# Performance work log

Hardware: AMD Instinct MI355X
Metric: run time of the kernel (lower is better)

Reference implementation:

```python
import jax, jax.numpy as jnp
import numpy as np

B, S, D, H, AD, E = 4, 2048, 1024, 2048, 128, 8

def _ln(x, g, b, eps=1e-5):
    m = jnp.mean(x, axis=-1, keepdims=True)
    v = jnp.var(x, axis=-1, keepdims=True)
    return (x - m) * jax.lax.rsqrt(v + eps) * g + b

def setup_inputs() -> dict:
    key = jax.random.key(0)
    ks = jax.random.split(key, 12)
    scale = 1.0 / D ** 0.5
    ascale = scale * 0.01
    ead = 0.01 / AD ** 0.5
    return {
        'x': jax.random.normal(ks[0], (B, S, D), jnp.float32),
        'expert_weights': jax.random.uniform(ks[1], (B, S, E), jnp.float32),
        'Wu': jax.random.normal(ks[2], (H, D), jnp.float32) * scale,
        'bu': jnp.zeros((H,), jnp.float32),
        'Wg': jax.random.normal(ks[3], (H, D), jnp.float32) * scale,
        'bg': jnp.zeros((H,), jnp.float32),
        'Wd': jax.random.normal(ks[4], (D, H), jnp.float32) * scale,
        'bd': jnp.zeros((D,), jnp.float32),
        'Wpre': jax.random.normal(ks[5], (AD, D), jnp.float32) * ascale,
        'bpre': jnp.zeros((AD,), jnp.float32),
        'Wpost': jax.random.normal(ks[6], (AD, H), jnp.float32) * ascale,
        'bpost': jnp.zeros((AD,), jnp.float32),
        'ln_g': jnp.ones((AD,), jnp.float32),
        'ln_b': jnp.zeros((AD,), jnp.float32),
        'Wap': jax.random.normal(ks[7], (H, AD), jnp.float32) * ascale,
        'A': jax.random.normal(ks[8], (E, AD, AD), jnp.float32) * ead,
        'eg': jnp.ones((E, AD), jnp.float32),
        'eb': jnp.zeros((E, AD), jnp.float32),
        'Wp': jax.random.normal(ks[9], (H, AD), jnp.float32) * ead,
        'Wo': jax.random.normal(ks[10], (D, H), jnp.float32) * ead,
    }

def reference(x, expert_weights, Wu, bu, Wg, bg, Wd, bd, Wpre, bpre, Wpost, bpost, ln_g, ln_b, Wap, A, eg, eb, Wp, Wo):
    # ---- SharedExpertMLP ----
    up = x @ Wu.T + bu                      # [B,S,H]
    gate = x @ Wg.T + bg
    hidden = jax.nn.silu(gate) * up
    adapt_in = _ln(x @ Wpre.T + bpre, ln_g, ln_b)        # [B,S,AD]
    adapt_out = _ln(hidden @ Wpost.T + bpost, ln_g, ln_b)
    aw = jnp.einsum('bsa,bta->bst', adapt_in, adapt_out)  # [B,S,S]
    aw = jax.nn.silu(jnp.clip(aw, -5.0, 5.0))
    adapt = jnp.einsum('bst,bta->bsa', aw, adapt_in)
    hidden = hidden + 0.1 * (adapt @ Wap.T)
    shared = hidden @ Wd.T + bd                           # [B,S,D]
    # ---- expert branch (vectorized over experts) ----
    pre = x @ Wpre.T + bpre                               # [B,S,AD] (no adapt_norm here, as in torch)
    h = jnp.einsum('bsa,eca->ebsc', pre, A)               # per-expert adapter linear
    h = _ln(h, eg[:, None, None, :], eb[:, None, None, :])
    wmask = jnp.where(expert_weights > 0, expert_weights, 0.0)  # [B,S,E]
    hw = jnp.einsum('ebsa,bse->bsa', h, wmask)            # weighted combine before shared projections
    Wc = Wo @ Wp                                          # [D,AD]: output_proj(expert_proj(.))
    contrib = hw @ Wc.T                                   # [B,S,D]
    # sum_i w_i * (shared + 0.1*mask_i*expert_i) = shared*sum(w) + 0.1*sum(w_i*expert_i)
    return shared * jnp.sum(expert_weights, axis=-1, keepdims=True) + 0.1 * contrib
```

## Files before the change

kernel.cpp:

```cpp
#include <hip/hip_runtime.h>
#include <math.h>

#define BB 4
#define SS 2048
#define DD 1024
#define HH 2048
#define AD 128
#define EE 8
#define MM (BB*SS)

typedef unsigned short u16;
typedef short bf16x8 __attribute__((ext_vector_type(8)));
typedef float f32x4 __attribute__((ext_vector_type(4)));

__device__ __forceinline__ float silu_f(float x){ return x / (1.f + __expf(-x)); }

__device__ __forceinline__ u16 f2bf(float f){
    union { float f; unsigned u; } c; c.f = f;
    unsigned r = (c.u + 0x7FFFu + ((c.u >> 16) & 1u)) >> 16;
    return (u16)r;
}
__device__ __forceinline__ float bf2f(u16 u){
    union { unsigned u; float f; } c; c.u = ((unsigned)u) << 16;
    return c.f;
}

__device__ __forceinline__ void gld16(const u16* g, u16* l){
    __builtin_amdgcn_global_load_lds((const __attribute__((address_space(1))) void*)g,
                                     (__attribute__((address_space(3))) void*)l, 16, 0, 0);
}

template<int EPI>
__global__ __launch_bounds__(256,2) void mfma_nt(
    const u16* __restrict__ A, const u16* __restrict__ B, void* Cv,
    int M, int N, int K, long sA, long sB, long sC,
    const float* __restrict__ bias, const float* __restrict__ rowscale,
    u16* Haux, float alpha)
{
    __shared__ __align__(16) u16 As[128*32];
    __shared__ __align__(16) u16 Bs[128*32];
    const int t = threadIdx.x;
    const int lane = t & 63;
    const int wv = t >> 6;
    const int m0 = blockIdx.y * 128, n0 = blockIdx.x * 128;
    const u16* Ab = A + (long)blockIdx.z * sA;
    const u16* Bb = B + (long)blockIdx.z * sB;
    const int srow = t >> 2, scol = (t & 3) * 8;
    const u16* ga0 = Ab + (long)(m0 + srow) * K + scol;
    const u16* ga1 = ga0 + 64L * K;
    const u16* gb0 = Bb + (long)(n0 + srow) * K + scol;
    const u16* gb1 = gb0 + 64L * K;
    u16* la0 = As + t * 8;  u16* la1 = As + 2048 + t * 8;
    u16* lb0 = Bs + t * 8;  u16* lb1 = Bs + 2048 + t * 8;
    const int fr = lane & 15, q = lane >> 4;
    const int wm = (wv & 1) * 64, wn = (wv >> 1) * 64;

    f32x4 acc[4][4] = {};
    for (int k0 = 0; k0 < K; k0 += 32) {
        gld16(ga0 + k0, la0);
        gld16(ga1 + k0, la1);
        gld16(gb0 + k0, lb0);
        gld16(gb1 + k0, lb1);
        __syncthreads();
        bf16x8 af[4], bfr[4];
        #pragma unroll
        for (int i = 0; i < 4; ++i) af[i]  = *(const bf16x8*)&As[(wm + i*16 + fr)*32 + q*8];
        #pragma unroll
        for (int i = 0; i < 4; ++i) bfr[i] = *(const bf16x8*)&Bs[(wn + i*16 + fr)*32 + q*8];
        #pragma unroll
        for (int mi = 0; mi < 4; ++mi)
            #pragma unroll
            for (int ni = 0; ni < 4; ++ni)
                acc[mi][ni] = __builtin_amdgcn_mfma_f32_16x16x32_bf16(af[mi], bfr[ni], acc[mi][ni], 0, 0, 0);
        __syncthreads();
    }

    float* Cf = (float*)Cv + (long)blockIdx.z * sC;
    u16*   Cb = (u16*)Cv   + (long)blockIdx.z * sC;
    u16*   Hb = Haux ? Haux + (long)blockIdx.z * sC : (u16*)0;
    #pragma unroll
    for (int mi = 0; mi < 4; ++mi) {
        #pragma unroll
        for (int ni = 0; ni < 4; ++ni) {
            const int col = n0 + wn + ni*16 + fr;
            #pragma unroll
            for (int r = 0; r < 4; ++r) {
                const int row = m0 + wm + mi*16 + q*4 + r;
                const long idx = (long)row * N + col;
                float v = acc[mi][ni][r];
                if (EPI == 0) {
                    if (bias) v += bias[col];
                    Cf[idx] = alpha * v;
                } else if (EPI == 2) {
                    v = fminf(fmaxf(v, -5.f), 5.f);
                    Cb[idx] = f2bf(silu_f(v));
                } else if (EPI == 3) {
                    Cb[idx] = f2bf(bf2f(Hb[idx]) + alpha * v);
                } else {
                    v = (v + bias[col]) * rowscale[row];
                    Cf[idx] += v;
                }
            }
        }
    }
}

__global__ __launch_bounds__(256,2) void mfma_sk(
    const u16* __restrict__ A, const u16* __restrict__ B, float* __restrict__ P,
    int M, int K, int S, long sA, long sB, long sC, long sSplit)
{
    __shared__ __align__(16) u16 As[128*32];
    __shared__ __align__(16) u16 Bs[128*32];
    const int t = threadIdx.x;
    const int lane = t & 63;
    const int wv = t >> 6;
    const int s = blockIdx.x;
    const int m0 = blockIdx.y * 128;
    const u16* Ab = A + (long)blockIdx.z * sA;
    const u16* Bb = B + (long)blockIdx.z * sB;
    const int srow = t >> 2, scol = (t & 3) * 8;
    const int Ks = K / S, kBeg = s * Ks;
    const u16* ga0 = Ab + (long)(m0 + srow) * K + scol + kBeg;
    const u16* ga1 = ga0 + 64L * K;
    const u16* gb0 = Bb + (long)srow * K + scol + kBeg;
    const u16* gb1 = gb0 + 64L * K;
    u16* la0 = As + t * 8;  u16* la1 = As + 2048 + t * 8;
    u16* lb0 = Bs + t * 8;  u16* lb1 = Bs + 2048 + t * 8;
    const int fr = lane & 15, q = lane >> 4;
    const int wm = (wv & 1) * 64, wn = (wv >> 1) * 64;

    f32x4 acc[4][4] = {};
    for (int k0 = 0; k0 < Ks; k0 += 32) {
        gld16(ga0 + k0, la0);
        gld16(ga1 + k0, la1);
        gld16(gb0 + k0, lb0);
        gld16(gb1 + k0, lb1);
        __syncthreads();
        bf16x8 af[4], bfr[4];
        #pragma unroll
        for (int i = 0; i < 4; ++i) af[i]  = *(const bf16x8*)&As[(wm + i*16 + fr)*32 + q*8];
        #pragma unroll
        for (int i = 0; i < 4; ++i) bfr[i] = *(const bf16x8*)&Bs[(wn + i*16 + fr)*32 + q*8];
        #pragma unroll
        for (int mi = 0; mi < 4; ++mi)
            #pragma unroll
            for (int ni = 0; ni < 4; ++ni)
                acc[mi][ni] = __builtin_amdgcn_mfma_f32_16x16x32_bf16(af[mi], bfr[ni], acc[mi][ni], 0, 0, 0);
        __syncthreads();
    }

    float* Pf = P + (long)s * sSplit + (long)blockIdx.z * sC;
    #pragma unroll
    for (int mi = 0; mi < 4; ++mi)
        #pragma unroll
        for (int ni = 0; ni < 4; ++ni) {
            const int col = wn + ni*16 + fr;
            #pragma unroll
            for (int r = 0; r < 4; ++r) {
                const int row = m0 + wm + mi*16 + q*4 + r;
                Pf[(long)row * 128 + col] = acc[mi][ni][r];
            }
        }
}

__global__ __launch_bounds__(256,2) void mfma_upgate(
    const u16* __restrict__ X, const u16* __restrict__ Wu_, const u16* __restrict__ Wg_,
    const float* __restrict__ bu, const float* __restrict__ bg, u16* __restrict__ H)
{
    __shared__ __align__(16) u16 Xs[128*32];
    __shared__ __align__(16) u16 Us[128*32];
    __shared__ __align__(16) u16 Gs[128*32];
    const int t = threadIdx.x, lane = t & 63, wv = t >> 6;
    const int m0 = blockIdx.y * 128, n0 = blockIdx.x * 128;
    const int srow = t >> 2, scol = (t & 3) * 8;
    const u16* gx0 = X   + (long)(m0 + srow) * DD + scol;
    const u16* gx1 = gx0 + 64L * DD;
    const u16* gu0 = Wu_ + (long)(n0 + srow) * DD + scol;
    const u16* gu1 = gu0 + 64L * DD;
    const u16* gg0 = Wg_ + (long)(n0 + srow) * DD + scol;
    const u16* gg1 = gg0 + 64L * DD;
    const int fr = lane & 15, q = lane >> 4;
    const int wm = (wv & 1) * 64, wn = (wv >> 1) * 64;

    f32x4 accu[4][4] = {};
    f32x4 accg[4][4] = {};
    for (int k0 = 0; k0 < DD; k0 += 32) {
        gld16(gx0 + k0, Xs + t*8);
        gld16(gx1 + k0, Xs + 2048 + t*8);
        gld16(gu0 + k0, Us + t*8);
        gld16(gu1 + k0, Us + 2048 + t*8);
        gld16(gg0 + k0, Gs + t*8);
        gld16(gg1 + k0, Gs + 2048 + t*8);
        __syncthreads();
        bf16x8 xf[4], uf[4], gf[4];
        #pragma unroll
        for (int i = 0; i < 4; ++i) {
            xf[i] = *(const bf16x8*)&Xs[(wm + i*16 + fr)*32 + q*8];
            uf[i] = *(const bf16x8*)&Us[(wn + i*16 + fr)*32 + q*8];
            gf[i] = *(const bf16x8*)&Gs[(wn + i*16 + fr)*32 + q*8];
        }
        #pragma unroll
        for (int mi = 0; mi < 4; ++mi)
            #pragma unroll
            for (int ni = 0; ni < 4; ++ni) {
                accu[mi][ni] = __builtin_amdgcn_mfma_f32_16x16x32_bf16(xf[mi], uf[ni], accu[mi][ni], 0, 0, 0);
                accg[mi][ni] = __builtin_amdgcn_mfma_f32_16x16x32_bf16(xf[mi], gf[ni], accg[mi][ni], 0, 0, 0);
            }
        __syncthreads();
    }
    #pragma unroll
    for (int mi = 0; mi < 4; ++mi) {
        #pragma unroll
        for (int ni = 0; ni < 4; ++ni) {
            const int col = n0 + wn + ni*16 + fr;
            #pragma unroll
            for (int r = 0; r < 4; ++r) {
                const int row = m0 + wm + mi*16 + q*4 + r;
                const float u = accu[mi][ni][r] + bu[col];
                const float g = accg[mi][ni][r] + bg[col];
                H[(long)row * HH + col] = f2bf(silu_f(g) * u);
            }
        }
    }
}

template<int S>
__global__ __launch_bounds__(128) void ln_reduce(
    const float* __restrict__ P, long sSplit, const float* __restrict__ bias,
    u16* __restrict__ raw, u16* __restrict__ ln_out,
    const float* __restrict__ g, const float* __restrict__ b)
{
    const int r = blockIdx.x, tid = threadIdx.x;
    float v = bias[tid];
    #pragma unroll
    for (int s = 0; s < S; ++s) v += P[(long)s * sSplit + (long)r * AD + tid];
    if (raw) raw[(long)r * AD + tid] = f2bf(v);
    __shared__ float red[AD], red2[AD];
    red[tid] = v; red2[tid] = v*v;
    __syncthreads();
    for (int s = 64; s > 0; s >>= 1) {
        if (tid < s) { red[tid] += red[tid+s]; red2[tid] += red2[tid+s]; }
        __syncthreads();
    }
    const float mean = red[0] * (1.f/AD);
    const float var  = red2[0] * (1.f/AD) - mean*mean;
    const float rs   = rsqrtf(var + 1e-5f);
    ln_out[(long)r * AD + tid] = f2bf((v - mean) * rs * g[tid] + b[tid]);
}

__global__ __launch_bounds__(256) void reduce_bf(
    const float* __restrict__ P, u16* __restrict__ out, long n4, int S, long stride4, float alpha)
{
    const long i = (long)blockIdx.x * 256 + threadIdx.x;
    if (i >= n4) return;
    float4 v = ((const float4*)P)[i];
    for (int s = 1; s < S; ++s) {
        const float4 w = ((const float4*)P)[i + s * stride4];
        v.x += w.x; v.y += w.y; v.z += w.z; v.w += w.w;
    }
    ushort4 o;
    o.x = f2bf(alpha*v.x); o.y = f2bf(alpha*v.y); o.z = f2bf(alpha*v.z); o.w = f2bf(alpha*v.w);
    ((ushort4*)out)[i] = o;
}

__global__ __launch_bounds__(128) void expert_combine(
    const float* __restrict__ h, const float* __restrict__ ew,
    const float* __restrict__ eg, const float* __restrict__ eb,
    u16* __restrict__ hw, float* __restrict__ sumw)
{
    const int m = blockIdx.x, tid = threadIdx.x;
    __shared__ float red[AD], red2[AD];
    __shared__ float wsh[EE];
    if (tid < EE) wsh[tid] = ew[(long)m * EE + tid];
    __syncthreads();
    float acc = 0.f;
    for (int e = 0; e < EE; ++e) {
        const float v = h[((long)e * MM + m) * AD + tid];
        red[tid] = v; red2[tid] = v*v;
        __syncthreads();
        for (int s = 64; s > 0; s >>= 1) {
            if (tid < s) { red[tid] += red[tid+s]; red2[tid] += red2[tid+s]; }
            __syncthreads();
        }
        const float mean = red[0] * (1.f/AD);
        const float var  = red2[0] * (1.f/AD) - mean*mean;
        const float rs   = rsqrtf(var + 1e-5f);
        const float nv   = (v - mean) * rs * eg[e*AD + tid] + eb[e*AD + tid];
        const float w    = wsh[e];
        acc += (w > 0.f ? w : 0.f) * nv;
        __syncthreads();
    }
    hw[(long)m * AD + tid] = f2bf(acc);
    if (tid == 0) {
        float s = 0.f;
        for (int e = 0; e < EE; ++e) s += wsh[e];
        sumw[m] = s;
    }
}

__global__ __launch_bounds__(256) void transpose_bf(
    const u16* __restrict__ in, u16* __restrict__ out, long sIn, long sOut)
{
    __shared__ u16 tile[32][33];
    in  += (long)blockIdx.z * sIn;
    out += (long)blockIdx.z * sOut;
    const int x0 = blockIdx.x * 32, y0 = blockIdx.y * 32;
    const int tx = threadIdx.x & 31, ty = threadIdx.x >> 5;
    #pragma unroll
    for (int j = 0; j < 4; ++j)
        tile[ty + j*8][tx] = in[(long)(y0 + ty + j*8) * AD + x0 + tx];
    __syncthreads();
    #pragma unroll
    for (int j = 0; j < 4; ++j)
        out[(long)(x0 + ty + j*8) * SS + y0 + tx] = tile[tx][ty + j*8];
}

struct Cvt5 { const float* in[5]; u16* out[5]; long cum[6]; };
__global__ __launch_bounds__(256) void cvt_pack(Cvt5 a)
{
    const long i = (long)blockIdx.x * 256 + threadIdx.x;
    if (i >= a.cum[5]) return;
    int s = 0;
    while (i >= a.cum[s+1]) ++s;
    const long j = i - a.cum[s];
    const float4 v = ((const float4*)a.in[s])[j];
    ushort4 o;
    o.x = f2bf(v.x); o.y = f2bf(v.y); o.z = f2bf(v.z); o.w = f2bf(v.w);
    ((ushort4*)a.out[s])[j] = o;
}

extern "C" void kernel_launch(void* const* d_in, const int* in_sizes, int n_in,
                              void* d_out, int out_size, void* d_ws, size_t ws_size,
                              hipStream_t stream) {
    const float* x    = (const float*)d_in[0];
    const float* ew   = (const float*)d_in[1];
    const float* Wu   = (const float*)d_in[2];
    const float* bu   = (const float*)d_in[3];
    const float* Wg   = (const float*)d_in[4];
    const float* bg   = (const float*)d_in[5];
    const float* Wd   = (const float*)d_in[6];
    const float* bd   = (const float*)d_in[7];
    const float* Wpre = (const float*)d_in[8];
    const float* bpre = (const float*)d_in[9];
    const float* Wpost= (const float*)d_in[10];
    const float* bpost= (const float*)d_in[11];
    const float* ln_g = (const float*)d_in[12];
    const float* ln_b = (const float*)d_in[13];
    const float* Wap  = (const float*)d_in[14];
    const float* Aex  = (const float*)d_in[15];
    const float* eg   = (const float*)d_in[16];
    const float* eb   = (const float*)d_in[17];
    const float* Wp   = (const float*)d_in[18];
    const float* Wo   = (const float*)d_in[19];
    float* out = (float*)d_out;

    char* p = (char*)d_ws;
    auto take = [&](long bytes) -> char* {
        char* r = p; p += (bytes + 255) & ~255L; return r;
    };
    u16* x_slot  = (u16*)take(16777216);
    u16* w1      = (u16*)take((long)HH*DD*2);
    u16* w2      = (u16*)take((long)HH*DD*2);
    u16* wpre    = (u16*)take((long)AD*DD*2);
    u16* aex     = (u16*)take((long)EE*AD*AD*2);
    u16* pre_bf  = (u16*)take((long)MM*AD*2);
    u16* ai_bf   = (u16*)take((long)MM*AD*2);
    char* shareA = take(33554432);
    u16* hw_bf   = (u16*)take((long)MM*AD*2);
    float* sumw  = (float*)take((long)MM*4);
    u16* hidden  = (u16*)take((long)MM*HH*2);

    u16* x_bf    = x_slot;
    u16* aiT     = x_slot;
    u16* adaptb  = aiT + 1048576;
    u16* pool    = adaptb + 1048576;
    u16* wpost_w = pool;
    u16* wo_bf   = wpost_w + 262144;
    u16* wp_bf   = wo_bf + 2097152;
    u16* wpT     = wp_bf + 262144;
    u16* wc_bf   = wpT + 262144;
    u16* ao_bf   = wc_bf + 131072;
    float* awaiP = (float*)pool;

    float* preP   = (float*)shareA;
    float* hbuf   = (float*)shareA;
    float* wcP    = (float*)shareA;
    float* wpostP = (float*)shareA;
    u16*   aw     = (u16*)shareA;

    {
        Cvt5 a;
        a.in[0]=x;    a.out[0]=x_bf;  long n0=(long)MM*DD/4;
        a.in[1]=Wu;   a.out[1]=w1;    long n1=(long)HH*DD/4;
        a.in[2]=Wg;   a.out[2]=w2;    long n2=(long)HH*DD/4;
        a.in[3]=Wpre; a.out[3]=wpre;  long n3=(long)AD*DD/4;
        a.in[4]=Aex;  a.out[4]=aex;   long n4=(long)EE*AD*AD/4;
        a.cum[0]=0; a.cum[1]=n0; a.cum[2]=n0+n1; a.cum[3]=n0+n1+n2;
        a.cum[4]=n0+n1+n2+n3; a.cum[5]=n0+n1+n2+n3+n4;
        cvt_pack<<<dim3((a.cum[5]+255)/256), 256, 0, stream>>>(a);
    }
    mfma_sk<<<dim3(4, MM/128, 1), 256, 0, stream>>>(
        x_bf, wpre, preP, MM, DD, 4, 0, 0, 0, (long)MM*AD);
    ln_reduce<4><<<dim3(MM), 128, 0, stream>>>(preP, (long)MM*AD, bpre, pre_bf, ai_bf, ln_g, ln_b);
    mfma_nt<0><<<dim3(1, MM/128, EE), 256, 0, stream>>>(pre_bf, aex, hbuf,
        MM, AD, AD, 0, (long)AD*AD, (long)MM*AD, nullptr, nullptr, nullptr, 1.f);
    expert_combine<<<dim3(MM), 128, 0, stream>>>(hbuf, ew, eg, eb, hw_bf, sumw);
    mfma_upgate<<<dim3(HH/128, MM/128, 1), 256, 0, stream>>>(x_bf, w1, w2, bu, bg, hidden);

    {
        Cvt5 a;
        a.in[0]=Wd;    a.out[0]=w1;      long n0=(long)DD*HH/4;
        a.in[1]=Wap;   a.out[1]=w2;      long n1=(long)HH*AD/4;
        a.in[2]=Wpost; a.out[2]=wpost_w; long n2=(long)AD*HH/4;
        a.in[3]=Wo;    a.out[3]=wo_bf;   long n3=(long)DD*HH/4;
        a.in[4]=Wp;    a.out[4]=wp_bf;   long n4=(long)HH*AD/4;
        a.cum[0]=0; a.cum[1]=n0; a.cum[2]=n0+n1; a.cum[3]=n0+n1+n2;
        a.cum[4]=n0+n1+n2+n3; a.cum[5]=n0+n1+n2+n3+n4;
        cvt_pack<<<dim3((a.cum[5]+255)/256), 256, 0, stream>>>(a);
    }
    transpose_bf<<<dim3(4,64,1), 256, 0, stream>>>(wp_bf, wpT, 0, 0);
    mfma_sk<<<dim3(8, DD/128, 1), 256, 0, stream>>>(
        wo_bf, wpT, wcP, DD, HH, 8, 0, 0, 0, (long)DD*AD);
    reduce_bf<<<dim3(((long)DD*AD/4+255)/256), 256, 0, stream>>>(
        wcP, wc_bf, (long)DD*AD/4, 8, (long)DD*AD/4, 1.f);
    mfma_nt<0><<<dim3(DD/128, MM/128, 1), 256, 0, stream>>>(hw_bf, wc_bf, out,
        MM, DD, AD, 0, 0, 0, nullptr, nullptr, nullptr, 0.1f);
    mfma_sk<<<dim3(8, MM/128, 1), 256, 0, stream>>>(
        hidden, wpost_w, wpostP, MM, HH, 8, 0, 0, 0, (long)MM*AD);
    ln_reduce<8><<<dim3(MM), 128, 0, stream>>>(wpostP, (long)MM*AD, bpost, nullptr, ao_bf, ln_g, ln_b);
    transpose_bf<<<dim3(4,64,4), 256, 0, stream>>>(ai_bf, aiT, (long)SS*AD, (long)AD*SS);
    mfma_nt<2><<<dim3(SS/128, SS/128, 4), 256, 0, stream>>>(ai_bf, ao_bf, aw,
        SS, SS, AD, (long)SS*AD, (long)SS*AD, (long)SS*SS, nullptr, nullptr, nullptr, 1.f);
    mfma_sk<<<dim3(2, SS/128, 4), 256, 0, stream>>>(
        aw, aiT, awaiP, SS, SS, 2, (long)SS*SS, (long)AD*SS, (long)SS*AD, (long)MM*AD);
    reduce_bf<<<dim3(((long)MM*AD/4+255)/256), 256, 0, stream>>>(
        awaiP, adaptb, (long)MM*AD/4, 2, (long)MM*AD/4, 1.f);
    mfma_nt<3><<<dim3(HH/128, MM/128, 1), 256, 0, stream>>>(adaptb, w2, hidden,
        MM, HH, AD, 0, 0, 0, nullptr, nullptr, hidden, 0.1f);
    mfma_nt<4><<<dim3(DD/128, MM/128, 1), 256, 0, stream>>>(hidden, w1, out,
        MM, DD, HH, 0, 0, 0, bd, sumw, nullptr, 1.f);
}
```

Before: 460.4 us.

## Fuse adapter attention, expert combine and final projection into flash-style kernels

Replaces the materialised SxS adapter-attention matrix with a flash-style kernel that computes clipped-SiLU scores into LDS and multiplies by adapt_in immediately. It also folds the adapt@Wap update into the final down-projection by precomputing Wd@Wap.T (pre-transposed) and concatenating it with the expert Wc, so one kernel does hidden@Wd plus a K=256 GEMM over [hw, sumw*adapt]. The per-expert linear, layernorm and weighted combine are fused into a single MFMA kernel without the fp32 intermediate. This removes large intermediate traffic and several launches, at the cost of reading operands directly from global memory without LDS staging in the new kernels and a changed rounding order.

```diff
diff --git a/kernel.cpp b/kernel.cpp
--- a/kernel.cpp
+++ b/kernel.cpp
@@ -8,6 +8,7 @@
 #define AD 128
 #define EE 8
 #define MM (BB*SS)
+#define PS 136
 
 typedef unsigned short u16;
 typedef short bf16x8 __attribute__((ext_vector_type(8)));
@@ -20,89 +21,10 @@
     unsigned r = (c.u + 0x7FFFu + ((c.u >> 16) & 1u)) >> 16;
     return (u16)r;
 }
-__device__ __forceinline__ float bf2f(u16 u){
-    union { unsigned u; float f; } c; c.u = ((unsigned)u) << 16;
-    return c.f;
-}
 
 __device__ __forceinline__ void gld16(const u16* g, u16* l){
     __builtin_amdgcn_global_load_lds((const __attribute__((address_space(1))) void*)g,
                                      (__attribute__((address_space(3))) void*)l, 16, 0, 0);
-}
-
-template<int EPI>
-__global__ __launch_bounds__(256,2) void mfma_nt(
-    const u16* __restrict__ A, const u16* __restrict__ B, void* Cv,
-    int M, int N, int K, long sA, long sB, long sC,
-    const float* __restrict__ bias, const float* __restrict__ rowscale,
-    u16* Haux, float alpha)
-{
-    __shared__ __align__(16) u16 As[128*32];
-    __shared__ __align__(16) u16 Bs[128*32];
-    const int t = threadIdx.x;
-    const int lane = t & 63;
-    const int wv = t >> 6;
-    const int m0 = blockIdx.y * 128, n0 = blockIdx.x * 128;
-    const u16* Ab = A + (long)blockIdx.z * sA;
-    const u16* Bb = B + (long)blockIdx.z * sB;
-    const int srow = t >> 2, scol = (t & 3) * 8;
-    const u16* ga0 = Ab + (long)(m0 + srow) * K + scol;
-    const u16* ga1 = ga0 + 64L * K;
-    const u16* gb0 = Bb + (long)(n0 + srow) * K + scol;
-    const u16* gb1 = gb0 + 64L * K;
-    u16* la0 = As + t * 8;  u16* la1 = As + 2048 + t * 8;
-    u16* lb0 = Bs + t * 8;  u16* lb1 = Bs + 2048 + t * 8;
-    const int fr = lane & 15, q = lane >> 4;
-    const int wm = (wv & 1) * 64, wn = (wv >> 1) * 64;
-
-    f32x4 acc[4][4] = {};
-    for (int k0 = 0; k0 < K; k0 += 32) {
-        gld16(ga0 + k0, la0);
-        gld16(ga1 + k0, la1);
-        gld16(gb0 + k0, lb0);
-        gld16(gb1 + k0, lb1);
-        __syncthreads();
-        bf16x8 af[4], bfr[4];
-        #pragma unroll
-        for (int i = 0; i < 4; ++i) af[i]  = *(const bf16x8*)&As[(wm + i*16 + fr)*32 + q*8];
-        #pragma unroll
-        for (int i = 0; i < 4; ++i) bfr[i] = *(const bf16x8*)&Bs[(wn + i*16 + fr)*32 + q*8];
-        #pragma unroll
-        for (int mi = 0; mi < 4; ++mi)
-            #pragma unroll
-            for (int ni = 0; ni < 4; ++ni)
-                acc[mi][ni] = __builtin_amdgcn_mfma_f32_16x16x32_bf16(af[mi], bfr[ni], acc[mi][ni], 0, 0, 0);
-        __syncthreads();
-    }
-
-    float* Cf = (float*)Cv + (long)blockIdx.z * sC;
-    u16*   Cb = (u16*)Cv   + (long)blockIdx.z * sC;
-    u16*   Hb = Haux ? Haux + (long)blockIdx.z * sC : (u16*)0;
-    #pragma unroll
-    for (int mi = 0; mi < 4; ++mi) {
-        #pragma unroll
-        for (int ni = 0; ni < 4; ++ni) {
-            const int col = n0 + wn + ni*16 + fr;
-            #pragma unroll
-            for (int r = 0; r < 4; ++r) {
-                const int row = m0 + wm + mi*16 + q*4 + r;
-                const long idx = (long)row * N + col;
-                float v = acc[mi][ni][r];
-                if (EPI == 0) {
-                    if (bias) v += bias[col];
-                    Cf[idx] = alpha * v;
-                } else if (EPI == 2) {
-                    v = fminf(fmaxf(v, -5.f), 5.f);
-                    Cb[idx] = f2bf(silu_f(v));
-                } else if (EPI == 3) {
-                    Cb[idx] = f2bf(bf2f(Hb[idx]) + alpha * v);
-                } else {
-                    v = (v + bias[col]) * rowscale[row];
-                    Cf[idx] += v;
-                }
-            }
-        }
-    }
 }
 
 __global__ __launch_bounds__(256,2) void mfma_sk(
@@ -224,6 +146,241 @@
     }
 }
 
+__global__ __launch_bounds__(256,2) void mfma_final(
+    const u16* __restrict__ Hh, const u16* __restrict__ Wd_,
+    const u16* __restrict__ Ac, const u16* __restrict__ Wcat,
+    const float* __restrict__ bd, const float* __restrict__ sumw,
+    float* __restrict__ out)
+{
+    __shared__ __align__(16) u16 As[128*32];
+    __shared__ __align__(16) u16 Bs[128*32];
+    const int t = threadIdx.x, lane = t & 63, wv = t >> 6;
+    const int m0 = blockIdx.y * 128, n0 = blockIdx.x * 128;
+    const int srow = t >> 2, scol = (t & 3) * 8;
+    const int fr = lane & 15, q = lane >> 4;
+    const int wm = (wv & 1) * 64, wn = (wv >> 1) * 64;
+    u16* la0 = As + t * 8;  u16* la1 = As + 2048 + t * 8;
+    u16* lb0 = Bs + t * 8;  u16* lb1 = Bs + 2048 + t * 8;
+
+    f32x4 acc[4][4] = {};
+    {
+        const u16* ga0 = Hh  + (long)(m0 + srow) * HH + scol;
+        const u16* ga1 = ga0 + 64L * HH;
+        const u16* gb0 = Wd_ + (long)(n0 + srow) * HH + scol;
+        const u16* gb1 = gb0 + 64L * HH;
+        for (int k0 = 0; k0 < HH; k0 += 32) {
+            gld16(ga0 + k0, la0);
+            gld16(ga1 + k0, la1);
+            gld16(gb0 + k0, lb0);
+            gld16(gb1 + k0, lb1);
+            __syncthreads();
+            bf16x8 af[4], bfr[4];
+            #pragma unroll
+            for (int i = 0; i < 4; ++i) af[i]  = *(const bf16x8*)&As[(wm + i*16 + fr)*32 + q*8];
+            #pragma unroll
+            for (int i = 0; i < 4; ++i) bfr[i] = *(const bf16x8*)&Bs[(wn + i*16 + fr)*32 + q*8];
+            #pragma unroll
+            for (int mi = 0; mi < 4; ++mi)
+                #pragma unroll
+                for (int ni = 0; ni < 4; ++ni)
+                    acc[mi][ni] = __builtin_amdgcn_mfma_f32_16x16x32_bf16(af[mi], bfr[ni], acc[mi][ni], 0, 0, 0);
+            __syncthreads();
+        }
+    }
+    f32x4 acc2[4][4] = {};
+    {
+        const u16* ga0 = Ac   + (long)(m0 + srow) * 256 + scol;
+        const u16* ga1 = ga0 + 64L * 256;
+        const u16* gb0 = Wcat + (long)(n0 + srow) * 256 + scol;
+        const u16* gb1 = gb0 + 64L * 256;
+        for (int k0 = 0; k0 < 256; k0 += 32) {
+            gld16(ga0 + k0, la0);
+            gld16(ga1 + k0, la1);
+            gld16(gb0 + k0, lb0);
+            gld16(gb1 + k0, lb1);
+            __syncthreads();
+            bf16x8 af[4], bfr[4];
+            #pragma unroll
+            for (int i = 0; i < 4; ++i) af[i]  = *(const bf16x8*)&As[(wm + i*16 + fr)*32 + q*8];
+            #pragma unroll
+            for (int i = 0; i < 4; ++i) bfr[i] = *(const bf16x8*)&Bs[(wn + i*16 + fr)*32 + q*8];
+            #pragma unroll
+            for (int mi = 0; mi < 4; ++mi)
+                #pragma unroll
+                for (int ni = 0; ni < 4; ++ni)
+                    acc2[mi][ni] = __builtin_amdgcn_mfma_f32_16x16x32_bf16(af[mi], bfr[ni], acc2[mi][ni], 0, 0, 0);
+            __syncthreads();
+        }
+    }
+    #pragma unroll
+    for (int mi = 0; mi < 4; ++mi)
+        #pragma unroll
+        for (int ni = 0; ni < 4; ++ni) {
+            const int col = n0 + wn + ni*16 + fr;
+            #pragma unroll
+            for (int r = 0; r < 4; ++r) {
+                const int row = m0 + wm + mi*16 + q*4 + r;
+                out[(long)row * DD + col] =
+                    sumw[row] * (acc[mi][ni][r] + bd[col]) + 0.1f * acc2[mi][ni][r];
+            }
+        }
+}
+
+__global__ __launch_bounds__(256,1) void expert_fused(
+    const u16* __restrict__ pre, const u16* __restrict__ aexp,
+    const float* __restrict__ ew, const float* __restrict__ eg,
+    const float* __restrict__ eb, u16* __restrict__ acat,
+    float* __restrict__ sumw)
+{
+    __shared__ float ewsh[128*8];
+    __shared__ float egsh[8*128], ebsh[8*128];
+    const int t = threadIdx.x, lane = t & 63, wv = t >> 6;
+    const int fr = lane & 15, q = lane >> 4;
+    const int wm = wv * 32;
+    const int m0 = blockIdx.x * 128;
+    {   const int row = t >> 1, j = (t & 1)*4;
+        *(float4*)&ewsh[row*8+j] = *(const float4*)&ew[(long)(m0+row)*EE + j]; }
+    {   const int e = t >> 5, c = (t & 31)*4;
+        *(float4*)&egsh[e*128+c] = *(const float4*)&eg[e*128+c];
+        *(float4*)&ebsh[e*128+c] = *(const float4*)&eb[e*128+c]; }
+    __syncthreads();
+
+    f32x4 hwacc[2][8] = {};
+    for (int e = 0; e < EE; ++e) {
+        f32x4 acc[2][8] = {};
+        const u16* Ae = aexp + (long)e * AD * AD;
+        #pragma unroll
+        for (int ks = 0; ks < 4; ++ks) {
+            bf16x8 af[2], bfr[8];
+            #pragma unroll
+            for (int mi = 0; mi < 2; ++mi)
+                af[mi] = *(const bf16x8*)&pre[(long)(m0 + wm + mi*16 + fr)*AD + ks*32 + q*8];
+            #pragma unroll
+            for (int ni = 0; ni < 8; ++ni)
+                bfr[ni] = *(const bf16x8*)&Ae[(long)(ni*16 + fr)*AD + ks*32 + q*8];
+            #pragma unroll
+            for (int mi = 0; mi < 2; ++mi)
+                #pragma unroll
+                for (int ni = 0; ni < 8; ++ni)
+                    acc[mi][ni] = __builtin_amdgcn_mfma_f32_16x16x32_bf16(af[mi], bfr[ni], acc[mi][ni], 0, 0, 0);
+        }
+        #pragma unroll
+        for (int mi = 0; mi < 2; ++mi)
+            #pragma unroll
+            for (int r = 0; r < 4; ++r) {
+                float s = 0.f, s2 = 0.f;
+                #pragma unroll
+                for (int ni = 0; ni < 8; ++ni) { const float v = acc[mi][ni][r]; s += v; s2 += v*v; }
+                #pragma unroll
+                for (int msk = 1; msk < 16; msk <<= 1) {
+                    s  += __shfl_xor(s,  msk, 64);
+                    s2 += __shfl_xor(s2, msk, 64);
+                }
+                const float mean = s * (1.f/128.f);
+                const float var  = s2 * (1.f/128.f) - mean*mean;
+                const float rs   = rsqrtf(var + 1e-5f);
+                const int rowl = wm + mi*16 + q*4 + r;
+                float w = ewsh[rowl*8 + e]; w = w > 0.f ? w : 0.f;
+                #pragma unroll
+                for (int ni = 0; ni < 8; ++ni) {
+                    const int col = ni*16 + fr;
+                    hwacc[mi][ni][r] += w * ((acc[mi][ni][r] - mean) * rs * egsh[e*128+col] + ebsh[e*128+col]);
+                }
+            }
+    }
+    #pragma unroll
+    for (int mi = 0; mi < 2; ++mi)
+        #pragma unroll
+        for (int r = 0; r < 4; ++r) {
+            const int rowl = wm + mi*16 + q*4 + r;
+            #pragma unroll
+            for (int ni = 0; ni < 8; ++ni)
+                acat[(long)(m0+rowl)*256 + ni*16 + fr] = f2bf(hwacc[mi][ni][r]);
+            if (fr == 0) {
+                float sw = 0.f;
+                #pragma unroll
+                for (int j = 0; j < 8; ++j) sw += ewsh[rowl*8 + j];
+                sumw[m0 + rowl] = sw;
+            }
+        }
+}
+
+__global__ __launch_bounds__(256,2) void flash_adapt(
+    const u16* __restrict__ ai, const u16* __restrict__ ao,
+    const u16* __restrict__ aiT, const float* __restrict__ sumw,
+    u16* __restrict__ acat)
+{
+    __shared__ __align__(16) u16 Psh[64*PS];
+    const int t = threadIdx.x, lane = t & 63, wv = t >> 6;
+    const int fr = lane & 15, q = lane >> 4;
+    const int wm = (wv & 1) * 32, wn = (wv >> 1) * 64;
+    const int b = blockIdx.y, q0 = blockIdx.x * 64;
+    const u16* aib  = ai  + (long)b * SS * AD;
+    const u16* aob  = ao  + (long)b * SS * AD;
+    const u16* aiTb = aiT + (long)b * AD * SS;
+
+    bf16x8 qf[2][4];
+    #pragma unroll
+    for (int mi = 0; mi < 2; ++mi)
+        #pragma unroll
+        for (int ks = 0; ks < 4; ++ks)
+            qf[mi][ks] = *(const bf16x8*)&aib[(long)(q0 + wm + mi*16 + fr)*AD + ks*32 + q*8];
+
+    f32x4 vacc[2][4] = {};
+    for (int tt = 0; tt < SS; tt += 128) {
+        f32x4 acc[2][4] = {};
+        #pragma unroll
+        for (int ks = 0; ks < 4; ++ks) {
+            bf16x8 bo[4];
+            #pragma unroll
+            for (int ni = 0; ni < 4; ++ni)
+                bo[ni] = *(const bf16x8*)&aob[(long)(tt + wn + ni*16 + fr)*AD + ks*32 + q*8];
+            #pragma unroll
+            for (int mi = 0; mi < 2; ++mi)
+                #pragma unroll
+                for (int ni = 0; ni < 4; ++ni)
+                    acc[mi][ni] = __builtin_amdgcn_mfma_f32_16x16x32_bf16(qf[mi][ks], bo[ni], acc[mi][ni], 0, 0, 0);
+        }
+        __syncthreads();
+        #pragma unroll
+        for (int mi = 0; mi < 2; ++mi)
+            #pragma unroll
+            for (int ni = 0; ni < 4; ++ni)
+                #pragma unroll
+                for (int r = 0; r < 4; ++r) {
+                    float v = acc[mi][ni][r];
+                    v = fminf(fmaxf(v, -5.f), 5.f);
+                    Psh[(wm + mi*16 + q*4 + r)*PS + wn + ni*16 + fr] = f2bf(silu_f(v));
+                }
+        __syncthreads();
+        #pragma unroll
+        for (int ks = 0; ks < 4; ++ks) {
+            bf16x8 pf[2], bi[4];
+            #pragma unroll
+            for (int mi = 0; mi < 2; ++mi)
+                pf[mi] = *(const bf16x8*)&Psh[(wm + mi*16 + fr)*PS + ks*32 + q*8];
+            #pragma unroll
+            for (int ni = 0; ni < 4; ++ni)
+                bi[ni] = *(const bf16x8*)&aiTb[(long)(wn + ni*16 + fr)*SS + tt + ks*32 + q*8];
+            #pragma unroll
+            for (int mi = 0; mi < 2; ++mi)
+                #pragma unroll
+                for (int ni = 0; ni < 4; ++ni)
+                    vacc[mi][ni] = __builtin_amdgcn_mfma_f32_16x16x32_bf16(pf[mi], bi[ni], vacc[mi][ni], 0, 0, 0);
+        }
+    }
+    #pragma unroll
+    for (int mi = 0; mi < 2; ++mi)
+        #pragma unroll
+        for (int r = 0; r < 4; ++r) {
+            const long grow = (long)b * SS + q0 + wm + mi*16 + q*4 + r;
+            const float sw = sumw[grow];
+            #pragma unroll
+            for (int ni = 0; ni < 4; ++ni)
+                acat[grow*256 + 128 + wn + ni*16 + fr] = f2bf(sw * vacc[mi][ni][r]);
+        }
+}
+
 template<int S>
 __global__ __launch_bounds__(128) void ln_reduce(
     const float* __restrict__ P, long sSplit, const float* __restrict__ bias,
@@ -248,54 +405,20 @@
     ln_out[(long)r * AD + tid] = f2bf((v - mean) * rs * g[tid] + b[tid]);
 }
 
-__global__ __launch_bounds__(256) void reduce_bf(
-    const float* __restrict__ P, u16* __restrict__ out, long n4, int S, long stride4, float alpha)
-{
-    const long i = (long)blockIdx.x * 256 + threadIdx.x;
-    if (i >= n4) return;
-    float4 v = ((const float4*)P)[i];
-    for (int s = 1; s < S; ++s) {
-        const float4 w = ((const float4*)P)[i + s * stride4];
+__global__ __launch_bounds__(256) void reduce_cat(
+    const float* __restrict__ P, u16* __restrict__ Wcat)
+{
+    const int i = blockIdx.x * 256 + threadIdx.x;
+    const int a4 = i & 31, z = (i >> 5) & 1, d = i >> 6;
+    const float* src = P + (long)z * (4L*DD*AD) + (long)d * AD + a4*4;
+    float4 v = *(const float4*)src;
+    #pragma unroll
+    for (int s = 1; s < 4; ++s) {
+        const float4 w = *(const float4*)(src + (long)s * DD * AD);
         v.x += w.x; v.y += w.y; v.z += w.z; v.w += w.w;
     }
-    ushort4 o;
-    o.x = f2bf(alpha*v.x); o.y = f2bf(alpha*v.y); o.z = f2bf(alpha*v.z); o.w = f2bf(alpha*v.w);
-    ((ushort4*)out)[i] = o;
-}
-
-__global__ __launch_bounds__(128) void expert_combine(
-    const float* __restrict__ h, const float* __restrict__ ew,
-    const float* __restrict__ eg, const float* __restrict__ eb,
-    u16* __restrict__ hw, float* __restrict__ sumw)
-{
-    const int m = blockIdx.x, tid = threadIdx.x;
-    __shared__ float red[AD], red2[AD];
-    __shared__ float wsh[EE];
-    if (tid < EE) wsh[tid] = ew[(long)m * EE + tid];
-    __syncthreads();
-    float acc = 0.f;
-    for (int e = 0; e < EE; ++e) {
-        const float v = h[((long)e * MM + m) * AD + tid];
-        red[tid] = v; red2[tid] = v*v;
-        __syncthreads();
-        for (int s = 64; s > 0; s >>= 1) {
-            if (tid < s) { red[tid] += red[tid+s]; red2[tid] += red2[tid+s]; }
-            __syncthreads();
-        }
-        const float mean = red[0] * (1.f/AD);
-        const float var  = red2[0] * (1.f/AD) - mean*mean;
-        const float rs   = rsqrtf(var + 1e-5f);
-        const float nv   = (v - mean) * rs * eg[e*AD + tid] + eb[e*AD + tid];
-        const float w    = wsh[e];
-        acc += (w > 0.f ? w : 0.f) * nv;
-        __syncthreads();
-    }
-    hw[(long)m * AD + tid] = f2bf(acc);
-    if (tid == 0) {
-        float s = 0.f;
-        for (int e = 0; e < EE; ++e) s += wsh[e];
-        sumw[m] = s;
-    }
+    ushort4 o; o.x=f2bf(v.x); o.y=f2bf(v.y); o.z=f2bf(v.z); o.w=f2bf(v.w);
+    ((ushort4*)Wcat)[(long)d*64 + z*32 + a4] = o;
 }
 
 __global__ __launch_bounds__(256) void transpose_bf(
@@ -359,42 +482,34 @@
         char* r = p; p += (bytes + 255) & ~255L; return r;
     };
     u16* x_slot  = (u16*)take(16777216);
-    u16* w1      = (u16*)take((long)HH*DD*2);
-    u16* w2      = (u16*)take((long)HH*DD*2);
+    u16* wslot   = (u16*)take((long)2*DD*HH*2);
     u16* wpre    = (u16*)take((long)AD*DD*2);
     u16* aex     = (u16*)take((long)EE*AD*AD*2);
     u16* pre_bf  = (u16*)take((long)MM*AD*2);
     u16* ai_bf   = (u16*)take((long)MM*AD*2);
     char* shareA = take(33554432);
-    u16* hw_bf   = (u16*)take((long)MM*AD*2);
+    u16* acat    = (u16*)take((long)MM*256*2);
     float* sumw  = (float*)take((long)MM*4);
     u16* hidden  = (u16*)take((long)MM*HH*2);
 
     u16* x_bf    = x_slot;
     u16* aiT     = x_slot;
-    u16* adaptb  = aiT + 1048576;
-    u16* pool    = adaptb + 1048576;
-    u16* wpost_w = pool;
-    u16* wo_bf   = wpost_w + 262144;
-    u16* wp_bf   = wo_bf + 2097152;
-    u16* wpT     = wp_bf + 262144;
-    u16* wc_bf   = wpT + 262144;
-    u16* ao_bf   = wc_bf + 131072;
-    float* awaiP = (float*)pool;
-
+    u16* wRaw    = aiT  + 1048576;
+    u16* wT      = wRaw + 524288;
+    u16* wpost_w = wT   + 524288;
+    u16* wcat    = wpost_w + 262144;
+    u16* ao_bf   = wcat + 262144;
+    float* wcP   = (float*)(ao_bf + 1048576);
     float* preP   = (float*)shareA;
-    float* hbuf   = (float*)shareA;
-    float* wcP    = (float*)shareA;
     float* wpostP = (float*)shareA;
-    u16*   aw     = (u16*)shareA;
 
     {
         Cvt5 a;
-        a.in[0]=x;    a.out[0]=x_bf;  long n0=(long)MM*DD/4;
-        a.in[1]=Wu;   a.out[1]=w1;    long n1=(long)HH*DD/4;
-        a.in[2]=Wg;   a.out[2]=w2;    long n2=(long)HH*DD/4;
-        a.in[3]=Wpre; a.out[3]=wpre;  long n3=(long)AD*DD/4;
-        a.in[4]=Aex;  a.out[4]=aex;   long n4=(long)EE*AD*AD/4;
+        a.in[0]=x;    a.out[0]=x_bf;            long n0=(long)MM*DD/4;
+        a.in[1]=Wu;   a.out[1]=wslot;           long n1=(long)HH*DD/4;
+        a.in[2]=Wg;   a.out[2]=wslot+(long)DD*HH; long n2=(long)HH*DD/4;
+        a.in[3]=Wpre; a.out[3]=wpre;            long n3=(long)AD*DD/4;
+        a.in[4]=Aex;  a.out[4]=aex;             long n4=(long)EE*AD*AD/4;
         a.cum[0]=0; a.cum[1]=n0; a.cum[2]=n0+n1; a.cum[3]=n0+n1+n2;
         a.cum[4]=n0+n1+n2+n3; a.cum[5]=n0+n1+n2+n3+n4;
         cvt_pack<<<dim3((a.cum[5]+255)/256), 256, 0, stream>>>(a);
@@ -402,41 +517,29 @@
     mfma_sk<<<dim3(4, MM/128, 1), 256, 0, stream>>>(
         x_bf, wpre, preP, MM, DD, 4, 0, 0, 0, (long)MM*AD);
     ln_reduce<4><<<dim3(MM), 128, 0, stream>>>(preP, (long)MM*AD, bpre, pre_bf, ai_bf, ln_g, ln_b);
-    mfma_nt<0><<<dim3(1, MM/128, EE), 256, 0, stream>>>(pre_bf, aex, hbuf,
-        MM, AD, AD, 0, (long)AD*AD, (long)MM*AD, nullptr, nullptr, nullptr, 1.f);
-    expert_combine<<<dim3(MM), 128, 0, stream>>>(hbuf, ew, eg, eb, hw_bf, sumw);
-    mfma_upgate<<<dim3(HH/128, MM/128, 1), 256, 0, stream>>>(x_bf, w1, w2, bu, bg, hidden);
-
+    expert_fused<<<dim3(MM/128), 256, 0, stream>>>(pre_bf, aex, ew, eg, eb, acat, sumw);
+    mfma_upgate<<<dim3(HH/128, MM/128, 1), 256, 0, stream>>>(
+        x_bf, wslot, wslot+(long)DD*HH, bu, bg, hidden);
     {
         Cvt5 a;
-        a.in[0]=Wd;    a.out[0]=w1;      long n0=(long)DD*HH/4;
-        a.in[1]=Wap;   a.out[1]=w2;      long n1=(long)HH*AD/4;
-        a.in[2]=Wpost; a.out[2]=wpost_w; long n2=(long)AD*HH/4;
-        a.in[3]=Wo;    a.out[3]=wo_bf;   long n3=(long)DD*HH/4;
-        a.in[4]=Wp;    a.out[4]=wp_bf;   long n4=(long)HH*AD/4;
+        a.in[0]=Wo;    a.out[0]=wslot;             long n0=(long)DD*HH/4;
+        a.in[1]=Wd;    a.out[1]=wslot+(long)DD*HH; long n1=(long)DD*HH/4;
+        a.in[2]=Wpost; a.out[2]=wpost_w;           long n2=(long)AD*HH/4;
+        a.in[3]=Wp;    a.out[3]=wRaw;              long n3=(long)HH*AD/4;
+        a.in[4]=Wap;   a.out[4]=wRaw+(long)HH*AD;  long n4=(long)HH*AD/4;
         a.cum[0]=0; a.cum[1]=n0; a.cum[2]=n0+n1; a.cum[3]=n0+n1+n2;
         a.cum[4]=n0+n1+n2+n3; a.cum[5]=n0+n1+n2+n3+n4;
         cvt_pack<<<dim3((a.cum[5]+255)/256), 256, 0, stream>>>(a);
     }
-    transpose_bf<<<dim3(4,64,1), 256, 0, stream>>>(wp_bf, wpT, 0, 0);
-    mfma_sk<<<dim3(8, DD/128, 1), 256, 0, stream>>>(
-        wo_bf, wpT, wcP, DD, HH, 8, 0, 0, 0, (long)DD*AD);
-    reduce_bf<<<dim3(((long)DD*AD/4+255)/256), 256, 0, stream>>>(
-        wcP, wc_bf, (long)DD*AD/4, 8, (long)DD*AD/4, 1.f);
-    mfma_nt<0><<<dim3(DD/128, MM/128, 1), 256, 0, stream>>>(hw_bf, wc_bf, out,
-        MM, DD, AD, 0, 0, 0, nullptr, nullptr, nullptr, 0.1f);
+    transpose_bf<<<dim3(4,64,2), 256, 0, stream>>>(wRaw, wT, (long)HH*AD, (long)AD*HH);
+    mfma_sk<<<dim3(4, DD/128, 2), 256, 0, stream>>>(
+        wslot, wT, wcP, DD, HH, 4, (long)DD*HH, (long)AD*HH, 4L*DD*AD, (long)DD*AD);
+    reduce_cat<<<dim3(256), 256, 0, stream>>>(wcP, wcat);
     mfma_sk<<<dim3(8, MM/128, 1), 256, 0, stream>>>(
         hidden, wpost_w, wpostP, MM, HH, 8, 0, 0, 0, (long)MM*AD);
     ln_reduce<8><<<dim3(MM), 128, 0, stream>>>(wpostP, (long)MM*AD, bpost, nullptr, ao_bf, ln_g, ln_b);
     transpose_bf<<<dim3(4,64,4), 256, 0, stream>>>(ai_bf, aiT, (long)SS*AD, (long)AD*SS);
-    mfma_nt<2><<<dim3(SS/128, SS/128, 4), 256, 0, stream>>>(ai_bf, ao_bf, aw,
-        SS, SS, AD, (long)SS*AD, (long)SS*AD, (long)SS*SS, nullptr, nullptr, nullptr, 1.f);
-    mfma_sk<<<dim3(2, SS/128, 4), 256, 0, stream>>>(
-        aw, aiT, awaiP, SS, SS, 2, (long)SS*SS, (long)AD*SS, (long)SS*AD, (long)MM*AD);
-    reduce_bf<<<dim3(((long)MM*AD/4+255)/256), 256, 0, stream>>>(
-        awaiP, adaptb, (long)MM*AD/4, 2, (long)MM*AD/4, 1.f);
-    mfma_nt<3><<<dim3(HH/128, MM/128, 1), 256, 0, stream>>>(adaptb, w2, hidden,
-        MM, HH, AD, 0, 0, 0, nullptr, nullptr, hidden, 0.1f);
-    mfma_nt<4><<<dim3(DD/128, MM/128, 1), 256, 0, stream>>>(hidden, w1, out,
-        MM, DD, HH, 0, 0, 0, bd, sumw, nullptr, 1.f);
-}
+    flash_adapt<<<dim3(SS/64, BB), 256, 0, stream>>>(ai_bf, ao_bf, aiT, sumw, acat);
+    mfma_final<<<dim3(DD/128, MM/128), 256, 0, stream>>>(
+        hidden, wslot+(long)DD*HH, acat, wcat, bd, sumw, out);
+}
```

Result: slower. 473.5 us (+2.9%).
